# Performance work log

Measured on AMD Instinct MI355X. Metric: run time of the kernel, lower is better.

## Reference

```python
import jax, jax.numpy as jnp
import numpy as np

B, S, D, H, DH = 2, 2048, 1024, 16, 64
R_ATTN, R_OUT, I, R_FC1, R_FC2 = 32, 512, 4096, 512, 512
LN_EPS = 1e-5


def _layernorm(x, g, b):
    mu = jnp.mean(x, axis=-1, keepdims=True)
    var = jnp.mean(jnp.square(x - mu), axis=-1, keepdims=True)
    return (x - mu) * jax.lax.rsqrt(var + LN_EPS) * g + b


def setup_inputs() -> dict:
    key = jax.random.key(0)
    ks = jax.random.split(key, 16)
    std = 0.02
    return {
        'hidden_states': jax.random.normal(ks[0], (B, S, D), jnp.float32),
        'ln1_g': jnp.ones((D,), jnp.float32),
        'ln1_b': jnp.zeros((D,), jnp.float32),
        'ln2_g': jnp.ones((D,), jnp.float32),
        'ln2_b': jnp.zeros((D,), jnp.float32),
        'q_U': jax.random.normal(ks[1], (D, H, R_ATTN), jnp.float32) * std,
        'q_V': jax.random.normal(ks[2], (H, R_ATTN, DH), jnp.float32) * std,
        'q_b': jnp.zeros((H, DH), jnp.float32),
        'k_U': jax.random.normal(ks[3], (D, H, R_ATTN), jnp.float32) * std,
        'k_V': jax.random.normal(ks[4], (H, R_ATTN, DH), jnp.float32) * std,
        'k_b': jnp.zeros((H, DH), jnp.float32),
        'v_U': jax.random.normal(ks[5], (D, H, R_ATTN), jnp.float32) * std,
        'v_V': jax.random.normal(ks[6], (H, R_ATTN, DH), jnp.float32) * std,
        'v_b': jnp.zeros((H, DH), jnp.float32),
        'out_U': jax.random.normal(ks[7], (D, R_OUT), jnp.float32) * std,
        'out_V': jax.random.normal(ks[8], (R_OUT, D), jnp.float32) * std,
        'out_b': jnp.zeros((D,), jnp.float32),
        'fc1_U': jax.random.normal(ks[9], (D, R_FC1), jnp.float32) * std,
        'fc1_V': jax.random.normal(ks[10], (R_FC1, I), jnp.float32) * std,
        'fc1_b': jnp.zeros((I,), jnp.float32),
        'fc2_U': jax.random.normal(ks[11], (I, R_FC2), jnp.float32) * std,
        'fc2_V': jax.random.normal(ks[12], (R_FC2, D), jnp.float32) * std,
        'fc2_b': jnp.zeros((D,), jnp.float32),
    }


def reference(hidden_states, ln1_g, ln1_b, ln2_g, ln2_b,
              q_U, q_V, q_b, k_U, k_V, k_b, v_U, v_V, v_b,
              out_U, out_V, out_b, fc1_U, fc1_V, fc1_b, fc2_U, fc2_V, fc2_b):
    Bx, Sx, Dx = hidden_states.shape
    scale = 1.0 / np.sqrt(DH).astype(np.float32)
    x = _layernorm(hidden_states, ln1_g, ln1_b)
    # low-rank per-head QKV: [B,S,D]x[D,H,r]x[H,r,dh] -> [B,H,S,dh]
    Q = jnp.einsum('bsd,dhr,hre->bhse', x, q_U, q_V) + q_b[None, :, None, :]
    K = jnp.einsum('bsd,dhr,hre->bhse', x, k_U, k_V) + k_b[None, :, None, :]
    V = jnp.einsum('bsd,dhr,hre->bhse', x, v_U, v_V) + v_b[None, :, None, :]
    scores = jnp.einsum('bhse,bhte->bhst', Q, K) * scale  # [B,H,S,S]
    causal = jnp.tril(jnp.ones((Sx, Sx), bool))
    neg_inf = jnp.finfo(scores.dtype).min
    scores = jnp.where(causal, scores, neg_inf)
    probs = jax.nn.softmax(scores, axis=-1)
    Y = jnp.einsum('bhst,bhte->bhse', probs, V)
    Y = Y.transpose(0, 2, 1, 3).reshape(Bx, Sx, Dx)  # merge heads
    Y = (Y @ out_U) @ out_V + out_b
    h = hidden_states + Y
    z = _layernorm(h, ln2_g, ln2_b)
    h1 = jax.nn.gelu((z @ fc1_U) @ fc1_V + fc1_b, approximate=False)
    h2 = (h1 @ fc2_U) @ fc2_V + fc2_b
    return h + h2
```

## Files before the change

### kernel.cpp

```cpp
#include <hip/hip_runtime.h>
#include <cstdint>
#include <cstddef>


#define NTOK 4096
#define DM   1024
#define SEQ  2048

typedef __attribute__((ext_vector_type(8))) __bf16 bf16x8;
typedef __attribute__((ext_vector_type(4))) float  f32x4;

__device__ __forceinline__ f32x4 mfma16(bf16x8 a, bf16x8 b, f32x4 c) {
  return __builtin_amdgcn_mfma_f32_16x16x32_bf16(a, b, c, 0, 0, 0);
}

__device__ __forceinline__ void gload16(const __bf16* g, __bf16* l) {
  __builtin_amdgcn_global_load_lds(
      (const __attribute__((address_space(1))) void*)g,
      (__attribute__((address_space(3))) void*)l, 16, 0, 0);
}

__global__ __launch_bounds__(256) void transpose_k(const float* __restrict__ in,
                                                   __bf16* __restrict__ out,
                                                   int R, int C) {
  __shared__ __bf16 t[32][33];
  int tx = threadIdx.x & 31, ty = threadIdx.x >> 5;
  int r0 = blockIdx.y * 32, c0 = blockIdx.x * 32;
#pragma unroll
  for (int i = 0; i < 32; i += 8)
    t[ty + i][tx] = (__bf16)in[(size_t)(r0 + ty + i) * C + c0 + tx];
  __syncthreads();
#pragma unroll
  for (int i = 0; i < 32; i += 8)
    out[(size_t)(c0 + ty + i) * R + r0 + tx] = t[tx][ty + i];
}

__global__ __launch_bounds__(256) void trans_v(const __bf16* __restrict__ qkv,
                                               __bf16* __restrict__ VT) {
  __shared__ __bf16 t[32][33];
  int tx = threadIdx.x & 31, ty = threadIdx.x >> 5;
  int bh = blockIdx.z, b = bh >> 4, h = bh & 15;
  int k0 = blockIdx.x * 32, d0 = blockIdx.y * 32;
#pragma unroll
  for (int i = 0; i < 32; i += 8)
    t[ty + i][tx] = qkv[(size_t)(b * SEQ + k0 + ty + i) * 3072 + 2048 + h * 64 + d0 + tx];
  __syncthreads();
#pragma unroll
  for (int i = 0; i < 32; i += 8)
    VT[(size_t)(bh * 64 + d0 + ty + i) * SEQ + k0 + tx] = t[tx][ty + i];
}

__global__ __launch_bounds__(256) void combine_uv(const float* __restrict__ qU,
                                                  const float* __restrict__ qV,
                                                  const float* __restrict__ kU,
                                                  const float* __restrict__ kV,
                                                  const float* __restrict__ vU,
                                                  const float* __restrict__ vV,
                                                  __bf16* __restrict__ WT) {
  __shared__ float sV[2048];
  int tid = threadIdx.x;
  int blk = blockIdx.x;
  int sel = blk >> 7;
  int rem = blk & 127;
  int h = rem >> 3, dc = rem & 7;
  int d0 = dc << 7;
  const float* U = sel == 0 ? qU : (sel == 1 ? kU : vU);
  const float* V = sel == 0 ? qV : (sel == 1 ? kV : vV);
  for (int i = tid; i < 2048; i += 256) sV[i] = V[h * 2048 + i];
  int d = d0 + (tid & 127);
  int eh = tid >> 7;
  const float* up = U + (size_t)d * 512 + h * 32;
  float u[32];
#pragma unroll
  for (int i = 0; i < 8; i++)
    *(float4*)&u[i * 4] = *(const float4*)(up + i * 4);
  __syncthreads();
  int e0 = eh * 32;
#pragma unroll
  for (int eg = 0; eg < 8; eg++) {
    float ax = 0.f, ay = 0.f, az = 0.f, aw = 0.f;
#pragma unroll
    for (int r = 0; r < 32; r++) {
      float4 v4 = *(const float4*)&sV[r * 64 + e0 + eg * 4];
      ax += u[r] * v4.x; ay += u[r] * v4.y;
      az += u[r] * v4.z; aw += u[r] * v4.w;
    }
    size_t prow = (size_t)(sel * 1024 + h * 64 + e0 + eg * 4) * 1024 + d;
    WT[prow]        = (__bf16)ax;
    WT[prow + 1024] = (__bf16)ay;
    WT[prow + 2048] = (__bf16)az;
    WT[prow + 3072] = (__bf16)aw;
  }
}

__global__ void concat3(const float* a, const float* b, const float* c, float* o) {
  int i = blockIdx.x * 256 + threadIdx.x;
  o[i] = (i < 1024) ? a[i] : (i < 2048 ? b[i - 1024] : c[i - 2048]);
}

__global__ __launch_bounds__(256) void cast_k(const float* __restrict__ in,
                                              __bf16* __restrict__ out, int n) {
  int i = blockIdx.x * 256 + threadIdx.x;
  if (i < n) out[i] = (__bf16)in[i];
}

template <int TWO>
__global__ __launch_bounds__(256) void ln_k(const float* __restrict__ x,
                                            const __bf16* __restrict__ x2,
                                            const float* __restrict__ g,
                                            const float* __restrict__ b,
                                            __bf16* __restrict__ out) {
  int row = blockIdx.x, tid = threadIdx.x;
  const float* xr = x + (size_t)row * DM;
  float v[4], s = 0.f, ss = 0.f;
#pragma unroll
  for (int i = 0; i < 4; i++) {
    int c = i * 256 + tid;
    v[i] = xr[c];
    if (TWO) v[i] += (float)x2[(size_t)row * DM + c];
    s += v[i]; ss += v[i] * v[i];
  }
#pragma unroll
  for (int m = 1; m < 64; m <<= 1) { s += __shfl_xor(s, m); ss += __shfl_xor(ss, m); }
  __shared__ float rs_[4], rss[4];
  if ((tid & 63) == 0) { rs_[tid >> 6] = s; rss[tid >> 6] = ss; }
  __syncthreads();
  s  = rs_[0] + rs_[1] + rs_[2] + rs_[3];
  ss = rss[0] + rss[1] + rss[2] + rss[3];
  float mu  = s * (1.f / 1024.f);
  float var = ss * (1.f / 1024.f) - mu * mu;
  float rstd = rsqrtf(var + 1e-5f);
#pragma unroll
  for (int i = 0; i < 4; i++) {
    int c = i * 256 + tid;
    out[(size_t)row * DM + c] = (__bf16)((v[i] - mu) * rstd * g[c] + b[c]);
  }
}

template <int EPI, int BN>
__global__ __launch_bounds__(256) void gemm_bt(const __bf16* __restrict__ A,
                                               const __bf16* __restrict__ BT,
                                               void* __restrict__ Cv,
                                               const float* __restrict__ bias,
                                               const float* __restrict__ resF,
                                               const __bf16* __restrict__ resB,
                                               int M, int N, int K) {
  constexpr int WR = (BN == 128) ? 4 : 2;
  __shared__ alignas(16) __bf16 la[2][128 * 32];
  __shared__ alignas(16) __bf16 lb[2][BN * 32];
  int tid = threadIdx.x;
  int lane = tid & 63;
  int wave = tid >> 6;
  int quad = lane >> 4, l15 = lane & 15;
  int gx = gridDim.x;
  int nwg = gx * gridDim.y;
  int flat = blockIdx.y * gx + blockIdx.x;
  if ((nwg & 7) == 0) flat = (flat & 7) * (nwg >> 3) + (flat >> 3);
  int bm = (flat / gx) * 128, bn = (flat % gx) * BN;
  int wm = (BN == 128) ? (wave >> 1) * 64 : wave * 32;
  int wn = (BN == 128) ? (wave & 1) * 64 : 0;
  int lr = lane >> 2, lc = (lane & 3) * 8;
  const __bf16* ga = A  + (size_t)(bm + wave * 32 + lr) * K + lc;
  const __bf16* gb = BT + (size_t)(bn + wave * (BN == 128 ? 32 : 16) + lr) * K + lc;
  f32x4 acc[WR][4] = {};

  auto stage = [&](int k0, int b) {
    __bf16* lab = &la[b][wave * 1024];
    gload16(ga + k0, lab);
    gload16(ga + (size_t)16 * K + k0, lab + 512);
    if (BN == 128) {
      __bf16* lbb = &lb[b][wave * 1024];
      gload16(gb + k0, lbb);
      gload16(gb + (size_t)16 * K + k0, lbb + 512);
    } else {
      gload16(gb + k0, &lb[b][wave * 512]);
    }
  };

  stage(0, 0);
  __syncthreads();
  for (int k0 = 0; k0 < K; k0 += 32) {
    int b = (k0 >> 5) & 1;
    if (k0 + 32 < K) stage(k0 + 32, b ^ 1);
    bf16x8 af[WR], bfr[4];
#pragma unroll
    for (int i = 0; i < WR; i++)
      af[i] = *(const bf16x8*)&la[b][(wm + i * 16 + l15) * 32 + quad * 8];
#pragma unroll
    for (int j = 0; j < 4; j++)
      bfr[j] = *(const bf16x8*)&lb[b][(wn + j * 16 + l15) * 32 + quad * 8];
#pragma unroll
    for (int i = 0; i < WR; i++)
#pragma unroll
      for (int j = 0; j < 4; j++)
        acc[i][j] = mfma16(af[i], bfr[j], acc[i][j]);
    __syncthreads();
  }
#pragma unroll
  for (int i = 0; i < WR; i++) {
#pragma unroll
    for (int j = 0; j < 4; j++) {
      int col = bn + wn + j * 16 + l15;
      float bv = bias ? bias[col] : 0.f;
#pragma unroll
      for (int r = 0; r < 4; r++) {
        int row = bm + wm + i * 16 + quad * 4 + r;
        size_t idx = (size_t)row * N + col;
        float v = acc[i][j][r] + bv;
        if (EPI == 0) {
          ((__bf16*)Cv)[idx] = (__bf16)v;
        } else if (EPI == 1) {
          v = 0.5f * v * (1.f + erff(v * 0.70710678118654752f));
          ((__bf16*)Cv)[idx] = (__bf16)v;
        } else {
          v += resF[idx] + (float)resB[idx];
          ((float*)Cv)[idx] = v;
        }
      }
    }
  }
}

__global__ __launch_bounds__(256) void gemm_bt64s(const __bf16* __restrict__ A,
                                                  const __bf16* __restrict__ BT,
                                                  __bf16* __restrict__ C,
                                                  int M, int N, int K) {
  __shared__ alignas(16) __bf16 la[2][64 * 32];
  __shared__ alignas(16) __bf16 lb[2][64 * 32];
  int tid = threadIdx.x;
  int lane = tid & 63;
  int wave = tid >> 6;
  int quad = lane >> 4, l15 = lane & 15;
  int gx = gridDim.x;
  int nwg = gx * gridDim.y;
  int flat = blockIdx.y * gx + blockIdx.x;
  if ((nwg & 7) == 0) flat = (flat & 7) * (nwg >> 3) + (flat >> 3);
  int bm = (flat / gx) * 64, bn = (flat % gx) * 64;
  int lr = tid >> 2, lc = (tid & 3) * 8;
  const __bf16* ga = A  + (size_t)(bm + lr) * K + lc;
  const __bf16* gb = BT + (size_t)(bn + lr) * K + lc;
  f32x4 acc[4] = {};

  auto stage = [&](int k0, int b) {
    gload16(ga + k0, &la[b][tid * 8]);
    gload16(gb + k0, &lb[b][tid * 8]);
  };

  stage(0, 0);
  __syncthreads();
  for (int k0 = 0; k0 < K; k0 += 32) {
    int b = (k0 >> 5) & 1;
    if (k0 + 32 < K) stage(k0 + 32, b ^ 1);
    bf16x8 af = *(const bf16x8*)&la[b][(wave * 16 + l15) * 32 + quad * 8];
    bf16x8 bfr[4];
#pragma unroll
    for (int j = 0; j < 4; j++)
      bfr[j] = *(const bf16x8*)&lb[b][(j * 16 + l15) * 32 + quad * 8];
#pragma unroll
    for (int j = 0; j < 4; j++)
      acc[j] = mfma16(af, bfr[j], acc[j]);
    __syncthreads();
  }
#pragma unroll
  for (int j = 0; j < 4; j++) {
    int col = bn + j * 16 + l15;
#pragma unroll
    for (int r = 0; r < 4; r++) {
      int row = bm + wave * 16 + quad * 4 + r;
      C[(size_t)row * N + col] = (__bf16)acc[j][r];
    }
  }
}

__global__ __launch_bounds__(256) void gemm_sk(const __bf16* __restrict__ A,
                                               const __bf16* __restrict__ BT,
                                               float* __restrict__ Cf,
                                               int M, int N, int K, int KS) {
  __shared__ alignas(16) __bf16 la[2][128 * 32];
  __shared__ alignas(16) __bf16 lb[2][128 * 32];
  int tid = threadIdx.x;
  int lane = tid & 63;
  int wave = tid >> 6;
  int quad = lane >> 4, l15 = lane & 15;
  int bm = blockIdx.y * 128, bn = blockIdx.x * 128;
  int wm = (wave >> 1) * 64, wn = (wave & 1) * 64;
  int klen = K / KS;
  int kbeg = blockIdx.z * klen, kend = kbeg + klen;
  int lr = lane >> 2, lc = (lane & 3) * 8;
  const __bf16* ga = A  + (size_t)(bm + wave * 32 + lr) * K + lc;
  const __bf16* gb = BT + (size_t)(bn + wave * 32 + lr) * K + lc;
  f32x4 acc[4][4] = {};

  auto stage = [&](int k0, int b) {
    __bf16* lab = &la[b][wave * 1024];
    __bf16* lbb = &lb[b][wave * 1024];
    gload16(ga + k0, lab);
    gload16(ga + (size_t)16 * K + k0, lab + 512);
    gload16(gb + k0, lbb);
    gload16(gb + (size_t)16 * K + k0, lbb + 512);
  };

  stage(kbeg, 0);
  __syncthreads();
  for (int k0 = kbeg; k0 < kend; k0 += 32) {
    int b = ((k0 - kbeg) >> 5) & 1;
    if (k0 + 32 < kend) stage(k0 + 32, b ^ 1);
    bf16x8 af[4], bfr[4];
#pragma unroll
    for (int i = 0; i < 4; i++)
      af[i] = *(const bf16x8*)&la[b][(wm + i * 16 + l15) * 32 + quad * 8];
#pragma unroll
    for (int j = 0; j < 4; j++)
      bfr[j] = *(const bf16x8*)&lb[b][(wn + j * 16 + l15) * 32 + quad * 8];
#pragma unroll
    for (int i = 0; i < 4; i++)
#pragma unroll
      for (int j = 0; j < 4; j++)
        acc[i][j] = mfma16(af[i], bfr[j], acc[i][j]);
    __syncthreads();
  }
#pragma unroll
  for (int i = 0; i < 4; i++)
#pragma unroll
    for (int j = 0; j < 4; j++) {
      int col = bn + wn + j * 16 + l15;
#pragma unroll
      for (int r = 0; r < 4; r++) {
        int row = bm + wm + i * 16 + quad * 4 + r;
        atomicAdd(&Cf[(size_t)row * N + col], acc[i][j][r]);
      }
    }
}

#define JOB(q, a, b) ((uint32_t)(q) | ((uint32_t)(a) << 8) | ((uint32_t)(b) << 16))
__device__ const uint32_t JOBTAB[24] = {
  JOB(7, 0, 16),  JOB(15, 0, 16), JOB(15, 16, 32),
  JOB(14, 0, 15), JOB(14, 15, 30),
  JOB(6, 0, 14),  JOB(13, 0, 14), JOB(13, 14, 28),
  JOB(12, 0, 13), JOB(12, 13, 26),
  JOB(5, 0, 12),  JOB(11, 0, 12), JOB(11, 12, 24),
  JOB(10, 0, 11), JOB(10, 11, 22),
  JOB(4, 0, 10),  JOB(9, 0, 10),  JOB(9, 10, 20),
  JOB(8, 0, 9),   JOB(8, 9, 18),
  JOB(3, 0, 8),   JOB(2, 0, 6),   JOB(1, 0, 4),   JOB(0, 0, 2),
};

__global__ __launch_bounds__(512, 6) void attn_k(const __bf16* __restrict__ QKV,
                                                 const __bf16* __restrict__ VT,
                                                 __bf16* __restrict__ Y,
                                                 float* __restrict__ Opart,
                                                 float* __restrict__ lpart) {
  const float SC = 0.18033688011112042f;
  const float C2 = 23.083120654223414f;
  __shared__ alignas(16) __bf16 lk[2][64 * 64];
  __shared__ alignas(16) __bf16 lv[2][64 * 64];
  __shared__ alignas(16) __bf16 P[8][16 * 72];
  int tid = threadIdx.x;
  int wave = tid >> 6, lane = tid & 63;
  int quad = lane >> 4, l15 = lane & 15;
  int bh = blockIdx.x & 31;
  int job = blockIdx.x >> 5;
  uint32_t jt = JOBTAB[job];
  int qb = jt & 255, kbeg = (jt >> 8) & 255, kend = (jt >> 16) & 255;
  bool split = qb >= 8;
  int b = bh >> 4, h = bh & 15;
  int q0w = (qb << 7) + wave * 16;
  const size_t RS = 3 * DM;
  const __bf16* base = QKV + (size_t)b * SEQ * RS;
  const __bf16* vtb  = VT + (size_t)bh * 64 * SEQ;

  const __bf16* qp = base + (size_t)(q0w + l15) * RS + h * 64 + quad * 8;
  bf16x8 aq0 = *(const bf16x8*)qp;
  bf16x8 aq1 = *(const bf16x8*)(qp + 32);

  int srow = tid >> 3, schunk = tid & 7;
  int sswz = (schunk ^ (srow & 7)) << 3;
  const __bf16* gk_src = base + (size_t)srow * RS + DM + h * 64 + sswz;
  const __bf16* gv_src = vtb + (size_t)srow * SEQ + sswz;

  int c0 = (quad ^ (l15 & 7)) << 3;
  int c1 = ((quad + 4) ^ (l15 & 7)) << 3;

  f32x4 zero4 = {0.f, 0.f, 0.f, 0.f};
  f32x4 O[4] = {zero4, zero4, zero4, zero4};
  float l_i[4] = {0.f, 0.f, 0.f, 0.f};

  int ntiles = kend - kbeg;

  gload16(gk_src + ((size_t)kbeg << 6) * RS, &lk[0][tid * 8]);
  gload16(gv_src + ((size_t)kbeg << 6),      &lv[0][tid * 8]);
  __syncthreads();

  for (int t = 0; t < ntiles; t++) {
    int kt = kbeg + t;
    int cur = t & 1;
    if (t + 1 < ntiles) {
      size_t kn = (size_t)(kt + 1) << 6;
      gload16(gk_src + kn * RS, &lk[cur ^ 1][tid * 8]);
      gload16(gv_src + kn,      &lv[cur ^ 1][tid * 8]);
    }
    int k0 = kt << 6;
    if (k0 <= q0w + 15) {
      f32x4 s[4] = {zero4, zero4, zero4, zero4};
#pragma unroll
      for (int gk = 0; gk < 4; gk++) {
        const __bf16* kr = &lk[cur][(gk * 16 + l15) * 64];
        bf16x8 kb0 = *(const bf16x8*)(kr + c0);
        bf16x8 kb1 = *(const bf16x8*)(kr + c1);
        s[gk] = mfma16(aq0, kb0, s[gk]);
        s[gk] = mfma16(aq1, kb1, s[gk]);
      }
      if (k0 + 63 <= q0w) {
#pragma unroll
        for (int r = 0; r < 4; r++) {
          float p0 = exp2f(fmaf(s[0][r], SC, -C2));
          float p1 = exp2f(fmaf(s[1][r], SC, -C2));
          float p2 = exp2f(fmaf(s[2][r], SC, -C2));
          float p3 = exp2f(fmaf(s[3][r], SC, -C2));
          l_i[r] += (p0 + p1) + (p2 + p3);
          int pr = quad * 4 + r;
          P[wave][pr * 72 + l15]      = (__bf16)p0;
          P[wave][pr * 72 + 16 + l15] = (__bf16)p1;
          P[wave][pr * 72 + 32 + l15] = (__bf16)p2;
          P[wave][pr * 72 + 48 + l15] = (__bf16)p3;
        }
      } else {
#pragma unroll
        for (int r = 0; r < 4; r++) {
          int qrow = q0w + quad * 4 + r;
          float p0 = (k0 + l15      <= qrow) ? exp2f(fmaf(s[0][r], SC, -C2)) : 0.f;
          float p1 = (k0 + 16 + l15 <= qrow) ? exp2f(fmaf(s[1][r], SC, -C2)) : 0.f;
          float p2 = (k0 + 32 + l15 <= qrow) ? exp2f(fmaf(s[2][r], SC, -C2)) : 0.f;
          float p3 = (k0 + 48 + l15 <= qrow) ? exp2f(fmaf(s[3][r], SC, -C2)) : 0.f;
          l_i[r] += (p0 + p1) + (p2 + p3);
          int pr = quad * 4 + r;
          P[wave][pr * 72 + l15]      = (__bf16)p0;
          P[wave][pr * 72 + 16 + l15] = (__bf16)p1;
          P[wave][pr * 72 + 32 + l15] = (__bf16)p2;
          P[wave][pr * 72 + 48 + l15] = (__bf16)p3;
        }
      }
      bf16x8 ap0 = *(const bf16x8*)&P[wave][l15 * 72 + quad * 8];
      bf16x8 ap1 = *(const bf16x8*)&P[wave][l15 * 72 + 32 + quad * 8];
#pragma unroll
      for (int nt = 0; nt < 4; nt++) {
        const __bf16* vr = &lv[cur][(nt * 16 + l15) * 64];
        bf16x8 bv0 = *(const bf16x8*)(vr + c0);
        bf16x8 bv1 = *(const bf16x8*)(vr + c1);
        O[nt] = mfma16(ap0, bv0, O[nt]);
        O[nt] = mfma16(ap1, bv1, O[nt]);
      }
    }
    __syncthreads();
  }

#pragma unroll
  for (int r = 0; r < 4; r++) {
    l_i[r] += __shfl_xor(l_i[r], 1);
    l_i[r] += __shfl_xor(l_i[r], 2);
    l_i[r] += __shfl_xor(l_i[r], 4);
    l_i[r] += __shfl_xor(l_i[r], 8);
  }
  if (!split) {
#pragma unroll
    for (int r = 0; r < 4; r++) {
      float inv = 1.f / l_i[r];
      size_t orow = (size_t)(b * SEQ + q0w + quad * 4 + r);
      __bf16* yp = Y + orow * DM + h * 64 + l15;
      yp[0]  = (__bf16)(O[0][r] * inv);
      yp[16] = (__bf16)(O[1][r] * inv);
      yp[32] = (__bf16)(O[2][r] * inv);
      yp[48] = (__bf16)(O[3][r] * inv);
    }
  } else {
#pragma unroll
    for (int r = 0; r < 4; r++) {
      int row = (q0w - 1024) + quad * 4 + r;
      float* op = Opart + (((size_t)bh << 10) + row) * 64 + l15;
      atomicAdd(op +  0, O[0][r]);
      atomicAdd(op + 16, O[1][r]);
      atomicAdd(op + 32, O[2][r]);
      atomicAdd(op + 48, O[3][r]);
      if (l15 == 0) atomicAdd(&lpart[((size_t)bh << 10) + row], l_i[r]);
    }
  }
}

__global__ __launch_bounds__(256) void norm_k(const float* __restrict__ Op,
                                              const float* __restrict__ lp,
                                              __bf16* __restrict__ Y) {
  int idx = blockIdx.x * 256 + threadIdx.x;
  int dh = idx & 63;
  int row = (idx >> 6) & 1023;
  int bh = idx >> 16;
  int b = bh >> 4, h = bh & 15;
  float inv = 1.f / lp[(bh << 10) + row];
  Y[(size_t)(b * SEQ + 1024 + row) * DM + h * 64 + dh] = (__bf16)(Op[idx] * inv);
}

extern "C" void kernel_launch(void* const* d_in, const int* in_sizes, int n_in,
                              void* d_out, int out_size, void* d_ws, size_t ws_size,
                              hipStream_t stream) {
  (void)in_sizes; (void)n_in; (void)out_size; (void)ws_size;
  const float* hidden = (const float*)d_in[0];
  const float* ln1_g  = (const float*)d_in[1];
  const float* ln1_b  = (const float*)d_in[2];
  const float* ln2_g  = (const float*)d_in[3];
  const float* ln2_b  = (const float*)d_in[4];
  const float* q_U = (const float*)d_in[5];
  const float* q_V = (const float*)d_in[6];
  const float* q_b = (const float*)d_in[7];
  const float* k_U = (const float*)d_in[8];
  const float* k_V = (const float*)d_in[9];
  const float* k_b = (const float*)d_in[10];
  const float* v_U = (const float*)d_in[11];
  const float* v_V = (const float*)d_in[12];
  const float* v_b = (const float*)d_in[13];
  const float* out_U = (const float*)d_in[14];
  const float* out_V = (const float*)d_in[15];
  const float* out_b = (const float*)d_in[16];
  const float* fc1_U = (const float*)d_in[17];
  const float* fc1_V = (const float*)d_in[18];
  const float* fc1_b = (const float*)d_in[19];
  const float* fc2_U = (const float*)d_in[20];
  const float* fc2_V = (const float*)d_in[21];
  const float* fc2_b = (const float*)d_in[22];

  const size_t MB = 1u << 20;
  char* ws = (char*)d_ws;
  __bf16* outUT = (__bf16*)(ws + 0 * MB);
  __bf16* outVT = (__bf16*)(ws + 1 * MB);
  __bf16* f1UT  = (__bf16*)(ws + 2 * MB);
  __bf16* f1VT  = (__bf16*)(ws + 3 * MB);
  __bf16* f2VT  = (__bf16*)(ws + 7 * MB);
  float*  bqkv  = (float*) (ws + 8 * MB);
  __bf16* wqkvT = (__bf16*)(ws + 9 * MB);
  __bf16* f2UT  = (__bf16*)(ws + 9 * MB);
  __bf16* xln   = (__bf16*)(ws + 15 * MB);
  __bf16* yattn = (__bf16*)(ws + 15 * MB);
  __bf16* zbuf  = (__bf16*)(ws + 15 * MB);
  float*  t3f32 = (float*) (ws + 15 * MB);
  __bf16* t3bf  = (__bf16*)(ws + 19 * MB);
  __bf16* qkv   = (__bf16*)(ws + 23 * MB);
  __bf16* h1c   = (__bf16*)(ws + 23 * MB);
  __bf16* tbuf  = (__bf16*)(ws + 43 * MB);
  __bf16* VT    = (__bf16*)(ws + 47 * MB);
  __bf16* hres  = (__bf16*)(ws + 47 * MB);
  float* Opart = (float*)d_out;
  float* lpart = (float*)d_out + 2097152;

  transpose_k<<<dim3(16, 32), 256, 0, stream>>>(out_U, outUT, 1024, 512);
  transpose_k<<<dim3(32, 16), 256, 0, stream>>>(out_V, outVT, 512, 1024);
  transpose_k<<<dim3(16, 32), 256, 0, stream>>>(fc1_U, f1UT, 1024, 512);
  transpose_k<<<dim3(128, 16), 256, 0, stream>>>(fc1_V, f1VT, 512, 4096);
  transpose_k<<<dim3(32, 16), 256, 0, stream>>>(fc2_V, f2VT, 512, 1024);
  combine_uv<<<384, 256, 0, stream>>>(q_U, q_V, k_U, k_V, v_U, v_V, wqkvT);
  concat3<<<12, 256, 0, stream>>>(q_b, k_b, v_b, bqkv);

  ln_k<0><<<NTOK, 256, 0, stream>>>(hidden, nullptr, ln1_g, ln1_b, xln);
  gemm_bt<0, 128><<<dim3(24, 32), 256, 0, stream>>>(xln, wqkvT, qkv, bqkv,
                                                    nullptr, nullptr, NTOK, 3072, 1024);
  transpose_k<<<dim3(16, 128), 256, 0, stream>>>(fc2_U, f2UT, 4096, 512);
  trans_v<<<dim3(64, 2, 32), 256, 0, stream>>>(qkv, VT);
  hipMemsetAsync(d_out, 0, (size_t)8519680, stream);
  attn_k<<<768, 512, 0, stream>>>(qkv, VT, yattn, Opart, lpart);
  norm_k<<<8192, 256, 0, stream>>>(Opart, lpart, yattn);
  gemm_bt64s<<<dim3(8, 64), 256, 0, stream>>>(yattn, outUT, tbuf, NTOK, 512, 1024);
  gemm_bt<0, 64><<<dim3(16, 32), 256, 0, stream>>>(tbuf, outVT, hres, out_b,
                                                   nullptr, nullptr, NTOK, 1024, 512);
  ln_k<1><<<NTOK, 256, 0, stream>>>(hidden, hres, ln2_g, ln2_b, zbuf);
  gemm_bt64s<<<dim3(8, 64), 256, 0, stream>>>(zbuf, f1UT, tbuf, NTOK, 512, 1024);
  for (int mc = 0; mc < 2; mc++) {
    __bf16* tchunk = tbuf + (size_t)mc * 2048 * 512;
    gemm_bt<1, 128><<<dim3(32, 16), 256, 0, stream>>>(tchunk, f1VT, h1c, fc1_b,
                                                      nullptr, nullptr, 2048, 4096, 512);
    hipMemsetAsync(t3f32, 0, (size_t)2048 * 512 * 4, stream);
    gemm_sk<<<dim3(4, 16, 4), 256, 0, stream>>>(h1c, f2UT, t3f32,
                                                2048, 512, 4096, 4);
    cast_k<<<4096, 256, 0, stream>>>(t3f32, t3bf + (size_t)mc * 2048 * 512,
                                     2048 * 512);
  }
  gemm_bt<3, 64><<<dim3(16, 32), 256, 0, stream>>>(t3bf, f2VT, (float*)d_out, fc2_b,
                                                   hidden, hres, NTOK, 1024, 512);
}
```

Measured before the change: 427.6 us.

## Swizzle GEMM LDS tiles and transpose attention score MFMA for vector P stores

All three bf16 GEMM kernels now XOR-swizzle the k-chunk column within LDS rows, on both the global-to-LDS load and the fragment reads, to cut LDS bank conflicts. The attention kernel swaps the MFMA operands for QK^T so each lane holds four consecutive keys for one query row. This lets P be written to LDS as one 4-wide bf16 vector per key group instead of scalar stores, and the row sum collapses to a single scalar per lane with fewer shuffles. The cost is extra XOR index arithmetic and a shuffle broadcast of the row sum at the end, plus some risk of mismatched swizzle or mask indexing.

New measurement: 423.4 us. Within noise of the previous version (-1.0%).

```diff
diff --git a/kernel.cpp b/kernel.cpp
--- a/kernel.cpp
+++ b/kernel.cpp
@@ -8,6 +8,7 @@
 #define SEQ  2048
 
 typedef __attribute__((ext_vector_type(8))) __bf16 bf16x8;
+typedef __attribute__((ext_vector_type(4))) __bf16 bf16x4;
 typedef __attribute__((ext_vector_type(4))) float  f32x4;
 
 __device__ __forceinline__ f32x4 mfma16(bf16x8 a, bf16x8 b, f32x4 c) {
@@ -159,9 +160,11 @@
   int bm = (flat / gx) * 128, bn = (flat % gx) * BN;
   int wm = (BN == 128) ? (wave >> 1) * 64 : wave * 32;
   int wn = (BN == 128) ? (wave & 1) * 64 : 0;
-  int lr = lane >> 2, lc = (lane & 3) * 8;
+  int lr = lane >> 2;
+  int lc = (((lane & 3) ^ ((lr >> 1) & 3))) * 8;
   const __bf16* ga = A  + (size_t)(bm + wave * 32 + lr) * K + lc;
   const __bf16* gb = BT + (size_t)(bn + wave * (BN == 128 ? 32 : 16) + lr) * K + lc;
+  int ksw = ((l15 >> 1) & 3) * 8;
   f32x4 acc[WR][4] = {};
 
   auto stage = [&](int k0, int b) {
@@ -185,10 +188,10 @@
     bf16x8 af[WR], bfr[4];
 #pragma unroll
     for (int i = 0; i < WR; i++)
-      af[i] = *(const bf16x8*)&la[b][(wm + i * 16 + l15) * 32 + quad * 8];
+      af[i] = *(const bf16x8*)&la[b][(wm + i * 16 + l15) * 32 + (quad * 8 ^ ksw)];
 #pragma unroll
     for (int j = 0; j < 4; j++)
-      bfr[j] = *(const bf16x8*)&lb[b][(wn + j * 16 + l15) * 32 + quad * 8];
+      bfr[j] = *(const bf16x8*)&lb[b][(wn + j * 16 + l15) * 32 + (quad * 8 ^ ksw)];
 #pragma unroll
     for (int i = 0; i < WR; i++)
 #pragma unroll
@@ -236,9 +239,11 @@
   int flat = blockIdx.y * gx + blockIdx.x;
   if ((nwg & 7) == 0) flat = (flat & 7) * (nwg >> 3) + (flat >> 3);
   int bm = (flat / gx) * 64, bn = (flat % gx) * 64;
-  int lr = tid >> 2, lc = (tid & 3) * 8;
+  int lr = tid >> 2;
+  int lc = (((tid & 3) ^ ((lr >> 1) & 3))) * 8;
   const __bf16* ga = A  + (size_t)(bm + lr) * K + lc;
   const __bf16* gb = BT + (size_t)(bn + lr) * K + lc;
+  int ksw = ((l15 >> 1) & 3) * 8;
   f32x4 acc[4] = {};
 
   auto stage = [&](int k0, int b) {
@@ -251,11 +256,11 @@
   for (int k0 = 0; k0 < K; k0 += 32) {
     int b = (k0 >> 5) & 1;
     if (k0 + 32 < K) stage(k0 + 32, b ^ 1);
-    bf16x8 af = *(const bf16x8*)&la[b][(wave * 16 + l15) * 32 + quad * 8];
+    bf16x8 af = *(const bf16x8*)&la[b][(wave * 16 + l15) * 32 + (quad * 8 ^ ksw)];
     bf16x8 bfr[4];
 #pragma unroll
     for (int j = 0; j < 4; j++)
-      bfr[j] = *(const bf16x8*)&lb[b][(j * 16 + l15) * 32 + quad * 8];
+      bfr[j] = *(const bf16x8*)&lb[b][(j * 16 + l15) * 32 + (quad * 8 ^ ksw)];
 #pragma unroll
     for (int j = 0; j < 4; j++)
       acc[j] = mfma16(af, bfr[j], acc[j]);
@@ -286,9 +291,11 @@
   int wm = (wave >> 1) * 64, wn = (wave & 1) * 64;
   int klen = K / KS;
   int kbeg = blockIdx.z * klen, kend = kbeg + klen;
-  int lr = lane >> 2, lc = (lane & 3) * 8;
+  int lr = lane >> 2;
+  int lc = (((lane & 3) ^ ((lr >> 1) & 3))) * 8;
   const __bf16* ga = A  + (size_t)(bm + wave * 32 + lr) * K + lc;
   const __bf16* gb = BT + (size_t)(bn + wave * 32 + lr) * K + lc;
+  int ksw = ((l15 >> 1) & 3) * 8;
   f32x4 acc[4][4] = {};
 
   auto stage = [&](int k0, int b) {
@@ -308,10 +315,10 @@
     bf16x8 af[4], bfr[4];
 #pragma unroll
     for (int i = 0; i < 4; i++)
-      af[i] = *(const bf16x8*)&la[b][(wm + i * 16 + l15) * 32 + quad * 8];
+      af[i] = *(const bf16x8*)&la[b][(wm + i * 16 + l15) * 32 + (quad * 8 ^ ksw)];
 #pragma unroll
     for (int j = 0; j < 4; j++)
-      bfr[j] = *(const bf16x8*)&lb[b][(wn + j * 16 + l15) * 32 + quad * 8];
+      bfr[j] = *(const bf16x8*)&lb[b][(wn + j * 16 + l15) * 32 + (quad * 8 ^ ksw)];
 #pragma unroll
     for (int i = 0; i < 4; i++)
 #pragma unroll
@@ -383,7 +390,7 @@
 
   f32x4 zero4 = {0.f, 0.f, 0.f, 0.f};
   f32x4 O[4] = {zero4, zero4, zero4, zero4};
-  float l_i[4] = {0.f, 0.f, 0.f, 0.f};
+  float l_i = 0.f;
 
   int ntiles = kend - kbeg;
 
@@ -407,37 +414,32 @@
         const __bf16* kr = &lk[cur][(gk * 16 + l15) * 64];
         bf16x8 kb0 = *(const bf16x8*)(kr + c0);
         bf16x8 kb1 = *(const bf16x8*)(kr + c1);
-        s[gk] = mfma16(aq0, kb0, s[gk]);
-        s[gk] = mfma16(aq1, kb1, s[gk]);
+        s[gk] = mfma16(kb0, aq0, s[gk]);
+        s[gk] = mfma16(kb1, aq1, s[gk]);
       }
       if (k0 + 63 <= q0w) {
 #pragma unroll
-        for (int r = 0; r < 4; r++) {
-          float p0 = exp2f(fmaf(s[0][r], SC, -C2));
-          float p1 = exp2f(fmaf(s[1][r], SC, -C2));
-          float p2 = exp2f(fmaf(s[2][r], SC, -C2));
-          float p3 = exp2f(fmaf(s[3][r], SC, -C2));
-          l_i[r] += (p0 + p1) + (p2 + p3);
-          int pr = quad * 4 + r;
-          P[wave][pr * 72 + l15]      = (__bf16)p0;
-          P[wave][pr * 72 + 16 + l15] = (__bf16)p1;
-          P[wave][pr * 72 + 32 + l15] = (__bf16)p2;
-          P[wave][pr * 72 + 48 + l15] = (__bf16)p3;
+        for (int gk = 0; gk < 4; gk++) {
+          float p0 = exp2f(fmaf(s[gk][0], SC, -C2));
+          float p1 = exp2f(fmaf(s[gk][1], SC, -C2));
+          float p2 = exp2f(fmaf(s[gk][2], SC, -C2));
+          float p3 = exp2f(fmaf(s[gk][3], SC, -C2));
+          l_i += (p0 + p1) + (p2 + p3);
+          bf16x4 pw = {(__bf16)p0, (__bf16)p1, (__bf16)p2, (__bf16)p3};
+          *(bf16x4*)&P[wave][l15 * 72 + gk * 16 + quad * 4] = pw;
         }
       } else {
-#pragma unroll
-        for (int r = 0; r < 4; r++) {
-          int qrow = q0w + quad * 4 + r;
-          float p0 = (k0 + l15      <= qrow) ? exp2f(fmaf(s[0][r], SC, -C2)) : 0.f;
-          float p1 = (k0 + 16 + l15 <= qrow) ? exp2f(fmaf(s[1][r], SC, -C2)) : 0.f;
-          float p2 = (k0 + 32 + l15 <= qrow) ? exp2f(fmaf(s[2][r], SC, -C2)) : 0.f;
-          float p3 = (k0 + 48 + l15 <= qrow) ? exp2f(fmaf(s[3][r], SC, -C2)) : 0.f;
-          l_i[r] += (p0 + p1) + (p2 + p3);
-          int pr = quad * 4 + r;
-          P[wave][pr * 72 + l15]      = (__bf16)p0;
-          P[wave][pr * 72 + 16 + l15] = (__bf16)p1;
-          P[wave][pr * 72 + 32 + l15] = (__bf16)p2;
-          P[wave][pr * 72 + 48 + l15] = (__bf16)p3;
+        int qrow = q0w + l15;
+#pragma unroll
+        for (int gk = 0; gk < 4; gk++) {
+          int kb = k0 + gk * 16 + quad * 4;
+          float p0 = (kb     <= qrow) ? exp2f(fmaf(s[gk][0], SC, -C2)) : 0.f;
+          float p1 = (kb + 1 <= qrow) ? exp2f(fmaf(s[gk][1], SC, -C2)) : 0.f;
+          float p2 = (kb + 2 <= qrow) ? exp2f(fmaf(s[gk][2], SC, -C2)) : 0.f;
+          float p3 = (kb + 3 <= qrow) ? exp2f(fmaf(s[gk][3], SC, -C2)) : 0.f;
+          l_i += (p0 + p1) + (p2 + p3);
+          bf16x4 pw = {(__bf16)p0, (__bf16)p1, (__bf16)p2, (__bf16)p3};
+          *(bf16x4*)&P[wave][l15 * 72 + gk * 16 + quad * 4] = pw;
         }
       }
       bf16x8 ap0 = *(const bf16x8*)&P[wave][l15 * 72 + quad * 8];
@@ -454,17 +456,12 @@
     __syncthreads();
   }
 
-#pragma unroll
-  for (int r = 0; r < 4; r++) {
-    l_i[r] += __shfl_xor(l_i[r], 1);
-    l_i[r] += __shfl_xor(l_i[r], 2);
-    l_i[r] += __shfl_xor(l_i[r], 4);
-    l_i[r] += __shfl_xor(l_i[r], 8);
-  }
+  l_i += __shfl_xor(l_i, 16);
+  l_i += __shfl_xor(l_i, 32);
   if (!split) {
 #pragma unroll
     for (int r = 0; r < 4; r++) {
-      float inv = 1.f / l_i[r];
+      float inv = 1.f / __shfl(l_i, quad * 4 + r);
       size_t orow = (size_t)(b * SEQ + q0w + quad * 4 + r);
       __bf16* yp = Y + orow * DM + h * 64 + l15;
       yp[0]  = (__bf16)(O[0][r] * inv);
@@ -481,8 +478,9 @@
       atomicAdd(op + 16, O[1][r]);
       atomicAdd(op + 32, O[2][r]);
       atomicAdd(op + 48, O[3][r]);
-      if (l15 == 0) atomicAdd(&lpart[((size_t)bh << 10) + row], l_i[r]);
-    }
+    }
+    if (quad == 0)
+      atomicAdd(&lpart[((size_t)bh << 10) + (q0w - 1024) + l15], l_i);
   }
 }
 
```
